# Kernel tuning notes

Hardware: AMD Instinct MI355X
Metric: run time of the kernel (lower is better)

## Reference

```python
import jax, jax.numpy as jnp
import numpy as np

B, C, N = 8, 512, 2048
C8 = C // 8


def setup_inputs() -> dict:
    key = jax.random.key(0)
    kx, kq, kk, kv, kg = jax.random.split(key, 5)
    return {
        "x": jax.random.normal(kx, (B, C, N), dtype=jnp.float32),
        "Wq": jax.random.normal(kq, (C8, C), dtype=jnp.float32) * (1.0 / np.sqrt(C)),
        "Wk": jax.random.normal(kk, (C8, C), dtype=jnp.float32) * (1.0 / np.sqrt(C)),
        "Wv": jax.random.normal(kv, (C, C), dtype=jnp.float32) * (1.0 / np.sqrt(C)),
        # torch init is gamma=0.0; use a small random value so the attention
        # branch contributes to the output.
        "gamma": jax.random.uniform(kg, (1,), dtype=jnp.float32),
    }


def reference(x, Wq, Wk, Wv, gamma):
    # 1x1 convs == per-position linear maps over channels
    f = jnp.einsum("oc,bcn->bon", Wq, x)   # [B, C/8, N]
    g = jnp.einsum("oc,bcn->bon", Wk, x)   # [B, C/8, N]
    h = jnp.einsum("oc,bcn->bon", Wv, x)   # [B, C,   N]
    # scores[b,n,m] = sum_c f[b,c,n] * g[b,c,m]  (unscaled, as in source)
    scores = jnp.einsum("bcn,bcm->bnm", f, g)  # [B, N, N]
    # softmax over dim=1 (the query-position axis) — atypical but faithful
    beta = jax.nn.softmax(scores, axis=1)
    # o = gamma * h @ beta + x
    o = gamma[0] * jnp.einsum("bcn,bnm->bcm", h, beta) + x
    return o
```

## Files before the change

kernel.cpp:

```cpp
#include <hip/hip_runtime.h>
#include <hip/hip_bf16.h>
#include <math.h>

#define NB 8
#define NC 512
#define NN 2048

typedef unsigned short u16;
typedef __attribute__((ext_vector_type(8))) short short8;
typedef __attribute__((ext_vector_type(4))) float f32x4;

__device__ __forceinline__ float bf16_to_f32(u16 v) {
  union { unsigned int u; float f; } c; c.u = ((unsigned int)v) << 16; return c.f;
}
__device__ __forceinline__ u16 f32_to_bf16(float f) {
  __hip_bfloat16 h = __float2bfloat16(f);
  union { __hip_bfloat16 h; u16 u; } c; c.h = h; return c.u;
}
__device__ __forceinline__ void split2(float v, unsigned short& hi, unsigned short& lo) {
  hi = f32_to_bf16(v);
  lo = f32_to_bf16(v - bf16_to_f32(hi));
}

__device__ __forceinline__ void gl_lds16(const void* g, void* l) {
  __builtin_amdgcn_global_load_lds(
      (const __attribute__((address_space(1))) unsigned int*)g,
      (__attribute__((address_space(3))) unsigned int*)l, 16, 0, 0);
}

__device__ __forceinline__ void stage128x32(const u16* __restrict__ src, size_t row_base,
                                            int selems, int k0, u16* lds, int tid) {
#pragma unroll
  for (int s = 0; s < 2; ++s) {
    int flat = s * 4096 + tid * 16;
    int row = flat >> 6;
    int kb  = flat & 63;
    const char* g = (const char*)(src + (row_base + row) * (size_t)selems + k0) + kb;
    u16* l = lds + s * 2048 + (tid & ~63) * 8;
    gl_lds16(g, l);
  }
}

__global__ __launch_bounds__(256)
void wsplit_kernel(const float* __restrict__ Wq, const float* __restrict__ Wk,
                   const float* __restrict__ Wv, u16* __restrict__ Whi,
                   u16* __restrict__ Wlo) {
  int idx = (blockIdx.x * 256 + threadIdx.x) * 4;
  int r = idx >> 9, c = idx & 511;
  const float* src;
  if (r < 64)       src = Wq + (size_t)r * NC + c;
  else if (r < 128) src = Wk + (size_t)(r - 64) * NC + c;
  else              src = Wv + (size_t)(r - 128) * NC + c;
  float4 v = *(const float4*)src;
  ushort4 hi, lo;
  split2(v.x, hi.x, lo.x); split2(v.y, hi.y, lo.y);
  split2(v.z, hi.z, lo.z); split2(v.w, hi.w, lo.w);
  *(ushort4*)&Whi[idx] = hi;
  *(ushort4*)&Wlo[idx] = lo;
}

__global__ __launch_bounds__(256)
void xsplit_kernel(const float* __restrict__ x, u16* __restrict__ xThi,
                   u16* __restrict__ xTlo) {
  const int b = blockIdx.z, c0 = blockIdx.y * 64, n0 = blockIdx.x * 64;
  __shared__ float t[64][65];
  const int tid = threadIdx.x, tx = tid & 15, ty = tid >> 4;
#pragma unroll
  for (int r = 0; r < 4; ++r) {
    int c = r * 16 + ty;
    float4 v = *(const float4*)&x[((size_t)b * NC + c0 + c) * NN + n0 + tx * 4];
    t[c][tx * 4 + 0] = v.x; t[c][tx * 4 + 1] = v.y;
    t[c][tx * 4 + 2] = v.z; t[c][tx * 4 + 3] = v.w;
  }
  __syncthreads();
#pragma unroll
  for (int r = 0; r < 4; ++r) {
    int n = r * 16 + ty;
    ushort4 hi, lo;
    split2(t[tx * 4 + 0][n], hi.x, lo.x);
    split2(t[tx * 4 + 1][n], hi.y, lo.y);
    split2(t[tx * 4 + 2][n], hi.z, lo.z);
    split2(t[tx * 4 + 3][n], hi.w, lo.w);
    size_t off = ((size_t)b * NN + n0 + n) * NC + c0 + tx * 4;
    *(ushort4*)&xThi[off] = hi;
    *(ushort4*)&xTlo[off] = lo;
  }
}

__global__ __launch_bounds__(256)
void proj_mfma_kernel(const u16* __restrict__ xThi, const u16* __restrict__ xTlo,
                      const u16* __restrict__ Whi, const u16* __restrict__ Wlo,
                      u16* __restrict__ fgThi, u16* __restrict__ fgTlo,
                      u16* __restrict__ hw) {
  const int b  = blockIdx.z;
  const int n0 = blockIdx.x * 128;
  const int r0 = blockIdx.y * 128;
  const bool fg = (r0 == 0);

  __shared__ u16 Wh[128 * 32], Wl[128 * 32], Xh[128 * 32], Xl[128 * 32];

  const int tid = threadIdx.x, wave = tid >> 6, lane = tid & 63;
  const int quad = lane >> 4, l16 = lane & 15;
  const int wa = (wave >> 1) * 64, wb = (wave & 1) * 64;
  const size_t xrow = (size_t)b * NN + n0;

  f32x4 acc[4][4];
#pragma unroll
  for (int i = 0; i < 4; ++i)
#pragma unroll
    for (int j = 0; j < 4; ++j) acc[i][j] = (f32x4){0.f, 0.f, 0.f, 0.f};

  for (int k0 = 0; k0 < NC; k0 += 32) {
    __syncthreads();
    stage128x32(Whi, r0, NC, k0, Wh, tid);
    stage128x32(xThi, xrow, NC, k0, Xh, tid);
    if (fg) {
      stage128x32(Wlo, r0, NC, k0, Wl, tid);
      stage128x32(xTlo, xrow, NC, k0, Xl, tid);
    }
    __syncthreads();

    if (fg) {
      short8 ah[4], al[4], bh[4], bl[4];
#pragma unroll
      for (int i = 0; i < 4; ++i) {
        ah[i] = *(short8*)&Wh[(wa + i * 16 + l16) * 32 + quad * 8];
        al[i] = *(short8*)&Wl[(wa + i * 16 + l16) * 32 + quad * 8];
      }
#pragma unroll
      for (int j = 0; j < 4; ++j) {
        bh[j] = *(short8*)&Xh[(wb + j * 16 + l16) * 32 + quad * 8];
        bl[j] = *(short8*)&Xl[(wb + j * 16 + l16) * 32 + quad * 8];
      }
#pragma unroll
      for (int i = 0; i < 4; ++i)
#pragma unroll
        for (int j = 0; j < 4; ++j) {
          acc[i][j] = __builtin_amdgcn_mfma_f32_16x16x32_bf16(ah[i], bh[j], acc[i][j], 0, 0, 0);
          acc[i][j] = __builtin_amdgcn_mfma_f32_16x16x32_bf16(ah[i], bl[j], acc[i][j], 0, 0, 0);
          acc[i][j] = __builtin_amdgcn_mfma_f32_16x16x32_bf16(al[i], bh[j], acc[i][j], 0, 0, 0);
        }
    } else {
      short8 ah[4], bh[4];
#pragma unroll
      for (int i = 0; i < 4; ++i)
        ah[i] = *(short8*)&Xh[(wa + i * 16 + l16) * 32 + quad * 8];
#pragma unroll
      for (int j = 0; j < 4; ++j)
        bh[j] = *(short8*)&Wh[(wb + j * 16 + l16) * 32 + quad * 8];
#pragma unroll
      for (int i = 0; i < 4; ++i)
#pragma unroll
        for (int j = 0; j < 4; ++j)
          acc[i][j] = __builtin_amdgcn_mfma_f32_16x16x32_bf16(ah[i], bh[j], acc[i][j], 0, 0, 0);
    }
  }

  if (fg) {
#pragma unroll
    for (int i = 0; i < 4; ++i)
#pragma unroll
      for (int j = 0; j < 4; ++j) {
        int rb = wa + i * 16 + quad * 4;
        int n  = n0 + wb + j * 16 + l16;
        ushort4 hi, lo;
        split2(acc[i][j][0], hi.x, lo.x); split2(acc[i][j][1], hi.y, lo.y);
        split2(acc[i][j][2], hi.z, lo.z); split2(acc[i][j][3], hi.w, lo.w);
        size_t off = ((size_t)b * NN + n) * 128 + rb;
        *(ushort4*)&fgThi[off] = hi;
        *(ushort4*)&fgTlo[off] = lo;
      }
  } else {
#pragma unroll
    for (int i = 0; i < 4; ++i)
#pragma unroll
      for (int j = 0; j < 4; ++j) {
        int nb = n0 + wa + i * 16 + quad * 4;
        int c  = r0 - 128 + wb + j * 16 + l16;
        ushort4 hi;
        hi.x = f32_to_bf16(acc[i][j][0]); hi.y = f32_to_bf16(acc[i][j][1]);
        hi.z = f32_to_bf16(acc[i][j][2]); hi.w = f32_to_bf16(acc[i][j][3]);
        *(ushort4*)&hw[((size_t)b * NC + c) * NN + nb] = hi;
      }
  }
}

__global__ __launch_bounds__(512)
void attn_out_kernel(const u16* __restrict__ fgThi, const u16* __restrict__ fgTlo,
                     const u16* __restrict__ hw, const float* __restrict__ x,
                     const float* __restrict__ gamma, float* __restrict__ out) {
  const int s = blockIdx.x;
  const int xcd = s & 7;
  const int t = s >> 3;
  const int mt = t & 15;
  const int hi5 = t >> 4;
  const int p = (hi5 << 3) | xcd;
  const int b = p >> 1;
  const int ch = p & 1;
  const int m0 = mt * 128;
  const int c0 = ch * 256;

  __shared__ u16 Fh[2][64 * 64], Fl[2][64 * 64];
  __shared__ u16 Hs[2][256 * 64];
  __shared__ u16 Ps[128 * 64];
  __shared__ float Dn[128];

  const int tid = threadIdx.x, wave = tid >> 6, lane = tid & 63;
  const int quad = lane >> 4, l16 = lane & 15;
  const int ws_n = (wave >> 2) * 32, ws_m = (wave & 3) * 32;
  const int wv_c = (wave >> 1) * 64, wv_m = (wave & 1) * 64;

  const size_t frow = (size_t)b * NN;
  const size_t hrow = (size_t)b * NC + c0;

  short8 gh[2][2], gl[2][2];
#pragma unroll
  for (int j = 0; j < 2; ++j)
#pragma unroll
    for (int k = 0; k < 2; ++k) {
      size_t o = (frow + m0 + ws_m + j * 16 + l16) * 128 + 64 + k * 32 + quad * 8;
      gh[j][k] = *(const short8*)&fgThi[o];
      gl[j][k] = *(const short8*)&fgTlo[o];
    }

  {
    int flat = tid * 16;
    int row = flat >> 7, chunk = (flat >> 4) & 7;
    int kb = ((chunk ^ (row & 7)) << 4);
    gl_lds16((const char*)(fgThi + (frow + row) * 128) + kb, Fh[0] + (tid & ~63) * 8);
    gl_lds16((const char*)(fgTlo + (frow + row) * 128) + kb, Fl[0] + (tid & ~63) * 8);
#pragma unroll
    for (int s2 = 0; s2 < 4; ++s2) {
      int f2 = s2 * 8192 + tid * 16;
      int r2 = f2 >> 7, c2 = (f2 >> 4) & 7;
      gl_lds16((const char*)(hw + (hrow + r2) * NN) + ((c2 ^ (r2 & 7)) << 4),
               Hs[0] + s2 * 4096 + (tid & ~63) * 8);
    }
  }
  __syncthreads();

  float dsum0 = 0.f, dsum1 = 0.f;
  f32x4 ao[4][4];
#pragma unroll
  for (int i = 0; i < 4; ++i)
#pragma unroll
    for (int j = 0; j < 4; ++j) ao[i][j] = (f32x4){0.f, 0.f, 0.f, 0.f};

  for (int it = 0; it < NN / 64; ++it) {
    const int cur = it & 1;
    if (it + 1 < NN / 64) {
      const int n1 = (it + 1) * 64;
      int flat = tid * 16;
      int row = flat >> 7, chunk = (flat >> 4) & 7;
      int kb = ((chunk ^ (row & 7)) << 4);
      gl_lds16((const char*)(fgThi + (frow + n1 + row) * 128) + kb,
               Fh[cur ^ 1] + (tid & ~63) * 8);
      gl_lds16((const char*)(fgTlo + (frow + n1 + row) * 128) + kb,
               Fl[cur ^ 1] + (tid & ~63) * 8);
#pragma unroll
      for (int s2 = 0; s2 < 4; ++s2) {
        int f2 = s2 * 8192 + tid * 16;
        int r2 = f2 >> 7, c2 = (f2 >> 4) & 7;
        gl_lds16((const char*)(hw + (hrow + r2) * NN + n1) + ((c2 ^ (r2 & 7)) << 4),
                 Hs[cur ^ 1] + s2 * 4096 + (tid & ~63) * 8);
      }
    }

    f32x4 as[2][2];
#pragma unroll
    for (int i = 0; i < 2; ++i)
#pragma unroll
      for (int j = 0; j < 2; ++j) as[i][j] = (f32x4){0.f, 0.f, 0.f, 0.f};
#pragma unroll
    for (int k = 0; k < 2; ++k) {
      short8 fh[2], fl[2];
#pragma unroll
      for (int i = 0; i < 2; ++i) {
        int rr = ws_n + i * 16 + l16;
        int ci = (((k * 4 + quad) ^ (rr & 7)) << 3);
        fh[i] = *(short8*)&Fh[cur][rr * 64 + ci];
        fl[i] = *(short8*)&Fl[cur][rr * 64 + ci];
      }
#pragma unroll
      for (int i = 0; i < 2; ++i)
#pragma unroll
        for (int j = 0; j < 2; ++j) {
          as[i][j] = __builtin_amdgcn_mfma_f32_16x16x32_bf16(fh[i], gh[j][k], as[i][j], 0, 0, 0);
          as[i][j] = __builtin_amdgcn_mfma_f32_16x16x32_bf16(fh[i], gl[j][k], as[i][j], 0, 0, 0);
          as[i][j] = __builtin_amdgcn_mfma_f32_16x16x32_bf16(fl[i], gh[j][k], as[i][j], 0, 0, 0);
        }
    }

#pragma unroll
    for (int j = 0; j < 2; ++j) {
      int m = ws_m + j * 16 + l16;
#pragma unroll
      for (int i = 0; i < 2; ++i) {
        float e0 = __expf(as[i][j][0]);
        float e1 = __expf(as[i][j][1]);
        float e2 = __expf(as[i][j][2]);
        float e3 = __expf(as[i][j][3]);
        if (j == 0) dsum0 += (e0 + e1) + (e2 + e3);
        else        dsum1 += (e0 + e1) + (e2 + e3);
        ushort4 pk;
        pk.x = f32_to_bf16(e0); pk.y = f32_to_bf16(e1);
        pk.z = f32_to_bf16(e2); pk.w = f32_to_bf16(e3);
        int nb = ws_n * 2 + i * 32 + quad * 8;
        int chunk = nb >> 4;
        int off = (nb & 15) >> 1;
        *(ushort4*)&Ps[m * 64 + ((chunk ^ (m & 7)) << 3) + off] = pk;
      }
    }

    asm volatile("s_waitcnt lgkmcnt(0)" ::: "memory");
    __builtin_amdgcn_s_barrier();

#pragma unroll
    for (int k = 0; k < 2; ++k) {
      short8 hh[4], pb[4];
#pragma unroll
      for (int i = 0; i < 4; ++i) {
        int rr = wv_c + i * 16 + l16;
        hh[i] = *(short8*)&Hs[cur][rr * 64 + ((((k * 4 + quad)) ^ (rr & 7)) << 3)];
      }
#pragma unroll
      for (int j = 0; j < 4; ++j) {
        int rm = wv_m + j * 16 + l16;
        pb[j] = *(short8*)&Ps[rm * 64 + ((((k * 4 + quad)) ^ (rm & 7)) << 3)];
      }
#pragma unroll
      for (int i = 0; i < 4; ++i)
#pragma unroll
        for (int j = 0; j < 4; ++j)
          ao[i][j] = __builtin_amdgcn_mfma_f32_16x16x32_bf16(hh[i], pb[j], ao[i][j], 0, 0, 0);
    }

    __syncthreads();
  }

  dsum0 += __shfl_xor(dsum0, 16); dsum0 += __shfl_xor(dsum0, 32);
  dsum1 += __shfl_xor(dsum1, 16); dsum1 += __shfl_xor(dsum1, 32);
  if (tid < 128) Dn[tid] = 0.f;
  __syncthreads();
  if (quad == 0) {
    atomicAdd(&Dn[ws_m + l16], dsum0);
    atomicAdd(&Dn[ws_m + 16 + l16], dsum1);
  }
  __syncthreads();

  const float g = gamma[0];
  float invd[4];
#pragma unroll
  for (int j = 0; j < 4; ++j)
    invd[j] = g / Dn[wv_m + j * 16 + l16];

#pragma unroll
  for (int i = 0; i < 4; ++i) {
#pragma unroll
    for (int j = 0; j < 4; ++j) {
      const int c = c0 + wv_c + i * 16 + quad * 4;
      const int m = m0 + wv_m + j * 16 + l16;
#pragma unroll
      for (int r = 0; r < 4; ++r) {
        size_t off = ((size_t)b * NC + c + r) * NN + m;
        out[off] = fmaf(invd[j], ao[i][j][r], x[off]);
      }
    }
  }
}

extern "C" void kernel_launch(void* const* d_in, const int* in_sizes, int n_in,
                              void* d_out, int out_size, void* d_ws, size_t ws_size,
                              hipStream_t stream) {
  const float* x     = (const float*)d_in[0];
  const float* Wq    = (const float*)d_in[1];
  const float* Wk    = (const float*)d_in[2];
  const float* Wv    = (const float*)d_in[3];
  const float* gamma = (const float*)d_in[4];
  float* out = (float*)d_out;

  char* ws = (char*)d_ws;
  u16*   xThi  = (u16*)ws;
  u16*   xTlo  = (u16*)(ws + 16777216);
  u16*   Whi   = (u16*)(ws + 33554432);
  u16*   Wlo   = (u16*)(ws + 34209792);
  u16*   fgThi = (u16*)(ws + 67108864);
  u16*   fgTlo = (u16*)(ws + 71303168);
  u16*   hw    = (u16*)(ws + 75497472);

  wsplit_kernel<<<dim3(320), 256, 0, stream>>>(Wq, Wk, Wv, Whi, Wlo);
  xsplit_kernel<<<dim3(NN / 64, NC / 64, NB), 256, 0, stream>>>(x, xThi, xTlo);
  proj_mfma_kernel<<<dim3(NN / 128, 5, NB), 256, 0, stream>>>(
      xThi, xTlo, Whi, Wlo, fgThi, fgTlo, hw);
  attn_out_kernel<<<dim3(256), 512, 0, stream>>>(fgThi, fgTlo, hw, x, gamma, out);
}
```

Before: 207.5 us.

## Double-buffer projection staging and software-pipeline the attention PV stage

The projection kernel gets double-buffered LDS tiles, so the next K-slice is loaded while the current one is consumed, and one barrier per iteration is dropped. The attention kernel double-buffers the probability tile P and defers the H·P MFMA by one iteration, so the score/exp work of tile it overlaps with the PV accumulation of tile it-1, with one barrier per iteration. This doubles LDS use for P and the projection tiles, which may lower occupancy, and the H tile is now loaded in the same iteration it is needed. That gives less time to hide that load's latency.

Measured after the change: 205.1 us. No clear change (-1.2%).

```diff
diff --git a/kernel.cpp b/kernel.cpp
--- a/kernel.cpp
+++ b/kernel.cpp
@@ -97,7 +97,7 @@
   const int r0 = blockIdx.y * 128;
   const bool fg = (r0 == 0);
 
-  __shared__ u16 Wh[128 * 32], Wl[128 * 32], Xh[128 * 32], Xl[128 * 32];
+  __shared__ u16 Wh[2][128 * 32], Wl[2][128 * 32], Xh[2][128 * 32], Xl[2][128 * 32];
 
   const int tid = threadIdx.x, wave = tid >> 6, lane = tid & 63;
   const int quad = lane >> 4, l16 = lane & 15;
@@ -110,27 +110,38 @@
 #pragma unroll
     for (int j = 0; j < 4; ++j) acc[i][j] = (f32x4){0.f, 0.f, 0.f, 0.f};
 
-  for (int k0 = 0; k0 < NC; k0 += 32) {
+  stage128x32(Whi, r0, NC, 0, Wh[0], tid);
+  stage128x32(xThi, xrow, NC, 0, Xh[0], tid);
+  if (fg) {
+    stage128x32(Wlo, r0, NC, 0, Wl[0], tid);
+    stage128x32(xTlo, xrow, NC, 0, Xl[0], tid);
+  }
+
+  const int KIT = NC / 32;
+  for (int ki = 0; ki < KIT; ++ki) {
     __syncthreads();
-    stage128x32(Whi, r0, NC, k0, Wh, tid);
-    stage128x32(xThi, xrow, NC, k0, Xh, tid);
-    if (fg) {
-      stage128x32(Wlo, r0, NC, k0, Wl, tid);
-      stage128x32(xTlo, xrow, NC, k0, Xl, tid);
-    }
-    __syncthreads();
+    if (ki + 1 < KIT) {
+      const int nb = (ki + 1) & 1, k1 = (ki + 1) * 32;
+      stage128x32(Whi, r0, NC, k1, Wh[nb], tid);
+      stage128x32(xThi, xrow, NC, k1, Xh[nb], tid);
+      if (fg) {
+        stage128x32(Wlo, r0, NC, k1, Wl[nb], tid);
+        stage128x32(xTlo, xrow, NC, k1, Xl[nb], tid);
+      }
+    }
+    const int cur = ki & 1;
 
     if (fg) {
       short8 ah[4], al[4], bh[4], bl[4];
 #pragma unroll
       for (int i = 0; i < 4; ++i) {
-        ah[i] = *(short8*)&Wh[(wa + i * 16 + l16) * 32 + quad * 8];
-        al[i] = *(short8*)&Wl[(wa + i * 16 + l16) * 32 + quad * 8];
+        ah[i] = *(short8*)&Wh[cur][(wa + i * 16 + l16) * 32 + quad * 8];
+        al[i] = *(short8*)&Wl[cur][(wa + i * 16 + l16) * 32 + quad * 8];
       }
 #pragma unroll
       for (int j = 0; j < 4; ++j) {
-        bh[j] = *(short8*)&Xh[(wb + j * 16 + l16) * 32 + quad * 8];
-        bl[j] = *(short8*)&Xl[(wb + j * 16 + l16) * 32 + quad * 8];
+        bh[j] = *(short8*)&Xh[cur][(wb + j * 16 + l16) * 32 + quad * 8];
+        bl[j] = *(short8*)&Xl[cur][(wb + j * 16 + l16) * 32 + quad * 8];
       }
 #pragma unroll
       for (int i = 0; i < 4; ++i)
@@ -144,10 +155,10 @@
       short8 ah[4], bh[4];
 #pragma unroll
       for (int i = 0; i < 4; ++i)
-        ah[i] = *(short8*)&Xh[(wa + i * 16 + l16) * 32 + quad * 8];
+        ah[i] = *(short8*)&Xh[cur][(wa + i * 16 + l16) * 32 + quad * 8];
 #pragma unroll
       for (int j = 0; j < 4; ++j)
-        bh[j] = *(short8*)&Wh[(wb + j * 16 + l16) * 32 + quad * 8];
+        bh[j] = *(short8*)&Wh[cur][(wb + j * 16 + l16) * 32 + quad * 8];
 #pragma unroll
       for (int i = 0; i < 4; ++i)
 #pragma unroll
@@ -202,7 +213,7 @@
 
   __shared__ u16 Fh[2][64 * 64], Fl[2][64 * 64];
   __shared__ u16 Hs[2][256 * 64];
-  __shared__ u16 Ps[128 * 64];
+  __shared__ u16 Ps[2][128 * 64];
   __shared__ float Dn[128];
 
   const int tid = threadIdx.x, wave = tid >> 6, lane = tid & 63;
@@ -229,15 +240,7 @@
     int kb = ((chunk ^ (row & 7)) << 4);
     gl_lds16((const char*)(fgThi + (frow + row) * 128) + kb, Fh[0] + (tid & ~63) * 8);
     gl_lds16((const char*)(fgTlo + (frow + row) * 128) + kb, Fl[0] + (tid & ~63) * 8);
-#pragma unroll
-    for (int s2 = 0; s2 < 4; ++s2) {
-      int f2 = s2 * 8192 + tid * 16;
-      int r2 = f2 >> 7, c2 = (f2 >> 4) & 7;
-      gl_lds16((const char*)(hw + (hrow + r2) * NN) + ((c2 ^ (r2 & 7)) << 4),
-               Hs[0] + s2 * 4096 + (tid & ~63) * 8);
-    }
-  }
-  __syncthreads();
+  }
 
   float dsum0 = 0.f, dsum1 = 0.f;
   f32x4 ao[4][4];
@@ -246,9 +249,12 @@
 #pragma unroll
     for (int j = 0; j < 4; ++j) ao[i][j] = (f32x4){0.f, 0.f, 0.f, 0.f};
 
-  for (int it = 0; it < NN / 64; ++it) {
+  const int NT = NN / 64;
+  for (int it = 0; it < NT; ++it) {
     const int cur = it & 1;
-    if (it + 1 < NN / 64) {
+    __syncthreads();
+
+    if (it + 1 < NT) {
       const int n1 = (it + 1) * 64;
       int flat = tid * 16;
       int row = flat >> 7, chunk = (flat >> 4) & 7;
@@ -257,12 +263,38 @@
                Fh[cur ^ 1] + (tid & ~63) * 8);
       gl_lds16((const char*)(fgTlo + (frow + n1 + row) * 128) + kb,
                Fl[cur ^ 1] + (tid & ~63) * 8);
+    }
+    {
+      const int n1 = it * 64;
 #pragma unroll
       for (int s2 = 0; s2 < 4; ++s2) {
         int f2 = s2 * 8192 + tid * 16;
         int r2 = f2 >> 7, c2 = (f2 >> 4) & 7;
         gl_lds16((const char*)(hw + (hrow + r2) * NN + n1) + ((c2 ^ (r2 & 7)) << 4),
-                 Hs[cur ^ 1] + s2 * 4096 + (tid & ~63) * 8);
+                 Hs[cur] + s2 * 4096 + (tid & ~63) * 8);
+      }
+    }
+
+    if (it > 0) {
+      const int prv = cur ^ 1;
+#pragma unroll
+      for (int k = 0; k < 2; ++k) {
+        short8 hh[4], pb[4];
+#pragma unroll
+        for (int i = 0; i < 4; ++i) {
+          int rr = wv_c + i * 16 + l16;
+          hh[i] = *(short8*)&Hs[prv][rr * 64 + ((((k * 4 + quad)) ^ (rr & 7)) << 3)];
+        }
+#pragma unroll
+        for (int j = 0; j < 4; ++j) {
+          int rm = wv_m + j * 16 + l16;
+          pb[j] = *(short8*)&Ps[prv][rm * 64 + ((((k * 4 + quad)) ^ (rm & 7)) << 3)];
+        }
+#pragma unroll
+        for (int i = 0; i < 4; ++i)
+#pragma unroll
+          for (int j = 0; j < 4; ++j)
+            ao[i][j] = __builtin_amdgcn_mfma_f32_16x16x32_bf16(hh[i], pb[j], ao[i][j], 0, 0, 0);
       }
     }
 
@@ -308,25 +340,26 @@
         int nb = ws_n * 2 + i * 32 + quad * 8;
         int chunk = nb >> 4;
         int off = (nb & 15) >> 1;
-        *(ushort4*)&Ps[m * 64 + ((chunk ^ (m & 7)) << 3) + off] = pk;
-      }
-    }
-
-    asm volatile("s_waitcnt lgkmcnt(0)" ::: "memory");
-    __builtin_amdgcn_s_barrier();
-
+        *(ushort4*)&Ps[cur][m * 64 + ((chunk ^ (m & 7)) << 3) + off] = pk;
+      }
+    }
+  }
+
+  __syncthreads();
+  {
+    const int prv = (NT - 1) & 1;
 #pragma unroll
     for (int k = 0; k < 2; ++k) {
       short8 hh[4], pb[4];
 #pragma unroll
       for (int i = 0; i < 4; ++i) {
         int rr = wv_c + i * 16 + l16;
-        hh[i] = *(short8*)&Hs[cur][rr * 64 + ((((k * 4 + quad)) ^ (rr & 7)) << 3)];
+        hh[i] = *(short8*)&Hs[prv][rr * 64 + ((((k * 4 + quad)) ^ (rr & 7)) << 3)];
       }
 #pragma unroll
       for (int j = 0; j < 4; ++j) {
         int rm = wv_m + j * 16 + l16;
-        pb[j] = *(short8*)&Ps[rm * 64 + ((((k * 4 + quad)) ^ (rm & 7)) << 3)];
+        pb[j] = *(short8*)&Ps[prv][rm * 64 + ((((k * 4 + quad)) ^ (rm & 7)) << 3)];
       }
 #pragma unroll
       for (int i = 0; i < 4; ++i)
@@ -334,8 +367,6 @@
         for (int j = 0; j < 4; ++j)
           ao[i][j] = __builtin_amdgcn_mfma_f32_16x16x32_bf16(hh[i], pb[j], ao[i][j], 0, 0, 0);
     }
-
-    __syncthreads();
   }
 
   dsum0 += __shfl_xor(dsum0, 16); dsum0 += __shfl_xor(dsum0, 32);
```
